# Kernel tuning notes

Hardware: AMD Instinct MI355X
Metric: run time of the kernel (lower is better)

Reference implementation:

```python
import jax, jax.numpy as jnp
import numpy as np

O = 100000   # num objects
R = 1000000  # num triplets
D = 128      # per-slot feature dim (input_dim[0]=input_dim[1]=input_dim[2])
SUM_D = 3 * D  # MLP in/out width
H = 256      # hidden_dim


def setup_inputs() -> dict:
    key = jax.random.key(0)
    k1, k2, k3, k4, k5 = jax.random.split(key, 5)
    object_feats = jax.random.normal(k1, (O, D), dtype=jnp.float32)
    relation_feats = jax.random.normal(k2, (R, D), dtype=jnp.float32)
    triplet = jax.random.randint(k3, (R, 3), 0, O, dtype=jnp.int64)
    # MLP: Linear(SUM_D->H) + ReLU + Linear(H->SUM_D), kaiming-normal init
    W1 = jax.random.normal(k4, (SUM_D, H), dtype=jnp.float32) * np.sqrt(2.0 / SUM_D)
    b1 = jnp.zeros((H,), dtype=jnp.float32)
    W2 = jax.random.normal(k5, (H, SUM_D), dtype=jnp.float32) * np.sqrt(2.0 / H)
    b2 = jnp.zeros((SUM_D,), dtype=jnp.float32)
    return {
        "object_feats": object_feats,
        "relation_feats": relation_feats,
        "W1": W1, "b1": b1, "W2": W2, "b2": b2,
        "triplet": triplet,
        "triplet_len": R,
    }


def reference(object_feats, relation_feats, W1, b1, W2, b2, triplet, triplet_len):
    t = triplet[:triplet_len]                      # [R, 3]
    subs = t[:, 0]                                 # [R]
    objs = t[:, 1]                                 # [R]
    # gather subj/obj feats, concat with relation feats -> [R, 3D]
    gcn_feat = jnp.concatenate(
        [object_feats[subs], relation_feats, object_feats[objs]], axis=1)
    # 2-layer MLP
    h = jax.nn.relu(gcn_feat @ W1 + b1)            # [R, H]
    out = h @ W2 + b2                              # [R, 3D]
    sub_out = out[:, :D]
    rel_out = out[:, D:-D]
    obj_out = out[:, -D:]
    # scatter-add back to object nodes, then mean by degree, plus residual
    acc = jnp.zeros_like(object_feats)
    acc = acc.at[subs].add(sub_out).at[objs].add(obj_out)   # [O, D]
    one = jnp.ones((triplet_len,), dtype=object_feats.dtype)
    cnt = jnp.zeros((object_feats.shape[0],), dtype=object_feats.dtype)
    cnt = cnt.at[subs].add(one).at[objs].add(one)           # [O]
    output_feat = acc / jnp.clip(cnt, 1.0)[:, None] + object_feats
    return (output_feat, rel_out, triplet, triplet_len)
```

## Files before the change

kernel.cpp:

```cpp
#include <hip/hip_runtime.h>

#define O_N 100000
#define R_N 1000000
#define DIM 128
#define SD 384
#define HD 256
#define BR 64
#define NT (R_N / BR)
#define OBJ8 (O_N * DIM / 8)

typedef __attribute__((ext_vector_type(8))) short short8;
typedef __attribute__((ext_vector_type(4))) float f32x4;

static __device__ __forceinline__ unsigned short f2bf(float x) {
    union { float f; unsigned int u; } v; v.f = x;
    unsigned int r = v.u + 0x7FFFu + ((v.u >> 16) & 1u);
    return (unsigned short)(r >> 16);
}
static __device__ __forceinline__ unsigned long long pack4(f32x4 v) {
    return  (unsigned long long)f2bf(v.x)
         | ((unsigned long long)f2bf(v.y) << 16)
         | ((unsigned long long)f2bf(v.z) << 32)
         | ((unsigned long long)f2bf(v.w) << 48);
}

__global__ void prep_weights(const float* __restrict__ W1, const float* __restrict__ W2,
                             unsigned short* __restrict__ W1T, unsigned short* __restrict__ W2T) {
    int i = blockIdx.x * 256 + threadIdx.x;
    if (i < SD * HD) {
        int h = i / SD, k = i - h * SD;
        W1T[i] = f2bf(W1[k * HD + h]);
    } else {
        int j = i - SD * HD;
        int c = j / HD, k = j - c * HD;
        W2T[j] = f2bf(W2[k * SD + c]);
    }
}

__global__ void conv_obj(const float* __restrict__ objF, unsigned short* __restrict__ objBF) {
    int i = blockIdx.x * 256 + threadIdx.x;
    if (i < OBJ8) {
        f32x4 v0 = ((const f32x4*)(objF + (size_t)i * 8))[0];
        f32x4 v1 = ((const f32x4*)(objF + (size_t)i * 8))[1];
        unsigned long long* dd = (unsigned long long*)(objBF + (size_t)i * 8);
        dd[0] = pack4(v0);
        dd[1] = pack4(v1);
    }
}

__global__ void trip_cnt(const int* __restrict__ trip, float* __restrict__ tripOut,
                         float* __restrict__ lenOut, float* __restrict__ cnt,
                         const int* __restrict__ tlen) {
    int i = blockIdx.x * 256 + threadIdx.x;
    if (i < R_N) {
        int s = trip[3 * i], o = trip[3 * i + 1], t2 = trip[3 * i + 2];
        tripOut[3 * i]     = (float)s;
        tripOut[3 * i + 1] = (float)o;
        tripOut[3 * i + 2] = (float)t2;
        atomicAdd(&cnt[min(max(s, 0), O_N - 1)], 1.0f);
        atomicAdd(&cnt[min(max(o, 0), O_N - 1)], 1.0f);
        if (i == 0) lenOut[0] = (float)tlen[0];
    }
}

__global__ __launch_bounds__(256, 3)
void mlp_kernel(const unsigned short* __restrict__ objBF, const float* __restrict__ relF,
                const unsigned short* __restrict__ W1T, const unsigned short* __restrict__ W2T,
                const float* __restrict__ b1, const float* __restrict__ b2,
                const int* __restrict__ trip,
                float* __restrict__ accB, float* __restrict__ relOut) {
    __shared__ __align__(16) unsigned char Hs[32768];
    __shared__ int idxBuf[128];

    const int tid  = threadIdx.x;
    const int lane = tid & 63;
    const int w    = tid >> 6;
    const int r0   = blockIdx.x * BR;
    const int l15  = lane & 15;
    const int l4   = lane >> 4;
    const int hW   = w * 64;
    const int cW   = w * 96;

    int subG[4], objG[4];
    #pragma unroll
    for (int nr = 0; nr < 4; ++nr) {
        int rr = r0 + nr * 16 + l15;
        subG[nr] = min(max(trip[3 * rr], 0), O_N - 1);
        objG[nr] = min(max(trip[3 * rr + 1], 0), O_N - 1);
    }

    f32x4 acc1[4][4];
    #pragma unroll
    for (int a = 0; a < 4; ++a)
        #pragma unroll
        for (int b = 0; b < 4; ++b) acc1[a][b] = (f32x4)0.0f;

    #define G1STEP(K0, BFR_EXPR)                                              \
    {                                                                         \
        const int k0 = (K0);                                                  \
        short8 af[4], bfr[4];                                                 \
        _Pragma("unroll")                                                     \
        for (int nr = 0; nr < 4; ++nr) { BFR_EXPR; }                          \
        _Pragma("unroll")                                                     \
        for (int mh = 0; mh < 4; ++mh)                                        \
            af[mh] = *(const short8*)(W1T + (hW + mh * 16 + l15) * SD + k0 + 8 * l4); \
        _Pragma("unroll")                                                     \
        for (int mh = 0; mh < 4; ++mh)                                        \
            _Pragma("unroll")                                                 \
            for (int nr = 0; nr < 4; ++nr)                                    \
                acc1[mh][nr] = __builtin_amdgcn_mfma_f32_16x16x32_bf16(       \
                    af[mh], bfr[nr], acc1[mh][nr], 0, 0, 0);                  \
    }

    #pragma unroll
    for (int ks = 0; ks < 4; ++ks)
        G1STEP(ks * 32,
            bfr[nr] = *(const short8*)(objBF + (size_t)subG[nr] * DIM + k0 + l4 * 8));
    #pragma unroll
    for (int ks = 4; ks < 8; ++ks)
        G1STEP(ks * 32,
            {
                const float* rp = relF + (size_t)(r0 + nr * 16 + l15) * DIM + (k0 - 128) + l4 * 8;
                f32x4 a0 = ((const f32x4*)rp)[0];
                f32x4 a1 = ((const f32x4*)rp)[1];
                union { unsigned long long q[2]; short8 v; } u;
                u.q[0] = pack4(a0); u.q[1] = pack4(a1);
                bfr[nr] = u.v;
            });
    #pragma unroll
    for (int ks = 8; ks < 12; ++ks)
        G1STEP(ks * 32,
            bfr[nr] = *(const short8*)(objBF + (size_t)objG[nr] * DIM + (k0 - 256) + l4 * 8));
    #undef G1STEP

    #pragma unroll
    for (int mh = 0; mh < 4; ++mh) {
        int hbase = hW + mh * 16 + 4 * l4;
        float bb0 = b1[hbase], bb1 = b1[hbase + 1], bb2 = b1[hbase + 2], bb3 = b1[hbase + 3];
        int hb   = hbase >> 3;
        int half = (hbase >> 2) & 1;
        #pragma unroll
        for (int nr = 0; nr < 4; ++nr) {
            int rel = nr * 16 + l15;
            unsigned long long pk =
                  (unsigned long long)f2bf(fmaxf(acc1[mh][nr][0] + bb0, 0.f))
                | ((unsigned long long)f2bf(fmaxf(acc1[mh][nr][1] + bb1, 0.f)) << 16)
                | ((unsigned long long)f2bf(fmaxf(acc1[mh][nr][2] + bb2, 0.f)) << 32)
                | ((unsigned long long)f2bf(fmaxf(acc1[mh][nr][3] + bb3, 0.f)) << 48);
            *(unsigned long long*)(Hs + rel * 512 + ((hb ^ (rel & 15)) << 4) + half * 8) = pk;
        }
    }
    if (tid < 2 * BR) {
        int rr = r0 + (tid & (BR - 1));
        idxBuf[tid] = min(max(trip[3 * rr + (tid >> 6)], 0), O_N - 1);
    }
    __syncthreads();

    f32x4 acc2[4][6];
    #pragma unroll
    for (int a = 0; a < 4; ++a)
        #pragma unroll
        for (int b = 0; b < 6; ++b) acc2[a][b] = (f32x4)0.0f;

    #pragma unroll
    for (int ks = 0; ks < 8; ++ks) {
        int k0 = ks * 32;
        short8 ha[4], wb[6];
        #pragma unroll
        for (int ma = 0; ma < 4; ++ma) {
            int rel = ma * 16 + l15;
            int hb  = (k0 >> 3) + l4;
            ha[ma] = *(const short8*)(Hs + rel * 512 + ((hb ^ (rel & 15)) << 4));
        }
        #pragma unroll
        for (int nb = 0; nb < 6; ++nb) {
            int c = cW + nb * 16 + l15;
            wb[nb] = *(const short8*)(W2T + c * HD + k0 + 8 * l4);
        }
        #pragma unroll
        for (int ma = 0; ma < 4; ++ma)
            #pragma unroll
            for (int nb = 0; nb < 6; ++nb)
                acc2[ma][nb] = __builtin_amdgcn_mfma_f32_16x16x32_bf16(
                    ha[ma], wb[nb], acc2[ma][nb], 0, 0, 0);
    }

    #pragma unroll
    for (int ma = 0; ma < 4; ++ma) {
        int rloc = ma * 16 + 4 * l4;
        int rg   = r0 + rloc;
        int subs[4], objs[4];
        #pragma unroll
        for (int q = 0; q < 4; ++q) {
            subs[q] = idxBuf[rloc + q];
            objs[q] = idxBuf[BR + rloc + q];
        }
        #pragma unroll
        for (int nb = 0; nb < 6; ++nb) {
            int c = cW + nb * 16 + l15;
            float b2v = b2[c];
            #pragma unroll
            for (int q = 0; q < 4; ++q) {
                float v = acc2[ma][nb][q] + b2v;
                if (c < DIM) {
                    atomicAdd(accB + (size_t)subs[q] * DIM + c, v);
                } else if (c < 2 * DIM) {
                    relOut[(size_t)(rg + q) * DIM + (c - DIM)] = v;
                } else {
                    atomicAdd(accB + (size_t)objs[q] * DIM + (c - 2 * DIM), v);
                }
            }
        }
    }
}

__global__ void finalize(const float* __restrict__ accB, const float* __restrict__ cnt,
                         const float* __restrict__ objF, float* __restrict__ outF) {
    int i = blockIdx.x * 256 + threadIdx.x;
    if (i < O_N * DIM / 4) {
        int row = i >> 5;
        float c = fmaxf(cnt[row], 1.0f);
        f32x4 a = ((const f32x4*)accB)[i];
        f32x4 o = ((const f32x4*)objF)[i];
        f32x4 r;
        r.x = a.x / c + o.x;
        r.y = a.y / c + o.y;
        r.z = a.z / c + o.z;
        r.w = a.w / c + o.w;
        ((f32x4*)outF)[i] = r;
    }
}

extern "C" void kernel_launch(void* const* d_in, const int* in_sizes, int n_in,
                              void* d_out, int out_size, void* d_ws, size_t ws_size,
                              hipStream_t stream) {
    const float* objF = (const float*)d_in[0];
    const float* relF = (const float*)d_in[1];
    const float* W1   = (const float*)d_in[2];
    const float* b1   = (const float*)d_in[3];
    const float* W2   = (const float*)d_in[4];
    const float* b2   = (const float*)d_in[5];
    const int*   trip = (const int*)d_in[6];
    const int*   tlen = (const int*)d_in[7];

    float* outF    = (float*)d_out;
    float* relOut  = outF + (size_t)O_N * DIM;
    float* tripOut = relOut + (size_t)R_N * DIM;
    float* lenOut  = tripOut + (size_t)R_N * 3;

    unsigned short* W1T = (unsigned short*)d_ws;
    unsigned short* W2T = W1T + SD * HD;
    float* accB = (float*)(W2T + SD * HD);
    float* cnt  = accB + (size_t)O_N * DIM;
    unsigned short* objBF = (unsigned short*)(cnt + O_N);

    (void)hipMemsetAsync(accB, 0, ((size_t)O_N * DIM + O_N) * sizeof(float), stream);
    prep_weights<<<(2 * SD * HD) / 256, 256, 0, stream>>>(W1, W2, W1T, W2T);
    conv_obj<<<(OBJ8 + 255) / 256, 256, 0, stream>>>(objF, objBF);
    trip_cnt<<<(R_N + 255) / 256, 256, 0, stream>>>(trip, tripOut, lenOut, cnt, tlen);
    mlp_kernel<<<NT, 256, 0, stream>>>(objBF, relF, W1T, W2T, b1, b2, trip, accB, relOut);
    finalize<<<(O_N * DIM / 4 + 255) / 256, 256, 0, stream>>>(accB, cnt, objF, outF);
}
```

Measured before the change: 1.620 ms.

## Split fused MLP into two kernels with LDS-staged gathered inputs

Splits the fused two-layer MLP kernel into gemm1 and gemm2 kernels. The bf16 hidden activations go to global memory, reusing the rel_out buffer as scratch, and are read back by the second kernel. The first kernel now stages the gathered subject/object rows into swizzled LDS with global_load_lds and stages the converted relation rows into LDS, replacing per-lane direct global loads inside the MFMA loop. The intent is to cut register pressure and improve occupancy per stage, and to make the gathers coalesced. The cost is an extra full write and read of the R×256 bf16 hidden tensor, plus one more kernel launch.

New measurement: 2.659 ms. 1.64x slower.

```diff
diff --git a/kernel.cpp b/kernel.cpp
--- a/kernel.cpp
+++ b/kernel.cpp
@@ -64,12 +64,11 @@
 }
 
 __global__ __launch_bounds__(256, 3)
-void mlp_kernel(const unsigned short* __restrict__ objBF, const float* __restrict__ relF,
-                const unsigned short* __restrict__ W1T, const unsigned short* __restrict__ W2T,
-                const float* __restrict__ b1, const float* __restrict__ b2,
-                const int* __restrict__ trip,
-                float* __restrict__ accB, float* __restrict__ relOut) {
-    __shared__ __align__(16) unsigned char Hs[32768];
+void gemm1_kernel(const unsigned short* __restrict__ objBF, const float* __restrict__ relF,
+                  const unsigned short* __restrict__ W1T, const float* __restrict__ b1,
+                  const int* __restrict__ trip, unsigned char* __restrict__ hbfB) {
+    __shared__ __align__(16) unsigned char Xso[32768];
+    __shared__ __align__(16) unsigned char Xsr[16384];
     __shared__ int idxBuf[128];
 
     const int tid  = threadIdx.x;
@@ -79,15 +78,39 @@
     const int l15  = lane & 15;
     const int l4   = lane >> 4;
     const int hW   = w * 64;
-    const int cW   = w * 96;
-
-    int subG[4], objG[4];
-    #pragma unroll
-    for (int nr = 0; nr < 4; ++nr) {
-        int rr = r0 + nr * 16 + l15;
-        subG[nr] = min(max(trip[3 * rr], 0), O_N - 1);
-        objG[nr] = min(max(trip[3 * rr + 1], 0), O_N - 1);
-    }
+
+    if (tid < 2 * BR) {
+        int rr = r0 + (tid & (BR - 1));
+        idxBuf[tid] = min(max(trip[3 * rr + (tid >> 6)], 0), O_N - 1);
+    }
+    __syncthreads();
+
+    #pragma unroll
+    for (int it = 0; it < 8; ++it) {
+        int a   = it * 256 + tid;
+        int row = a >> 5;
+        int q   = a & 31;
+        int u   = q ^ (row & 15);
+        const unsigned short* src =
+            objBF + (size_t)((q < 16) ? idxBuf[row] : idxBuf[BR + row]) * DIM + (u & 15) * 8;
+        __builtin_amdgcn_global_load_lds(
+            (const __attribute__((address_space(1))) void*)src,
+            (__attribute__((address_space(3))) void*)(Xso + it * 4096 + w * 1024),
+            16, 0, 0);
+    }
+    #pragma unroll
+    for (int it = 0; it < 4; ++it) {
+        int a2  = it * 256 + tid;
+        int row = a2 >> 4;
+        int j   = a2 & 15;
+        const float* rp = relF + (size_t)(r0 + row) * DIM + j * 8;
+        f32x4 v0 = ((const f32x4*)rp)[0];
+        f32x4 v1 = ((const f32x4*)rp)[1];
+        union { unsigned long long q[2]; short8 v; } u;
+        u.q[0] = pack4(v0); u.q[1] = pack4(v1);
+        *(short8*)(Xsr + row * 256 + ((j ^ (row & 15)) << 4)) = u.v;
+    }
+    __syncthreads();
 
     f32x4 acc1[4][4];
     #pragma unroll
@@ -95,43 +118,30 @@
         #pragma unroll
         for (int b = 0; b < 4; ++b) acc1[a][b] = (f32x4)0.0f;
 
-    #define G1STEP(K0, BFR_EXPR)                                              \
-    {                                                                         \
-        const int k0 = (K0);                                                  \
-        short8 af[4], bfr[4];                                                 \
-        _Pragma("unroll")                                                     \
-        for (int nr = 0; nr < 4; ++nr) { BFR_EXPR; }                          \
-        _Pragma("unroll")                                                     \
-        for (int mh = 0; mh < 4; ++mh)                                        \
-            af[mh] = *(const short8*)(W1T + (hW + mh * 16 + l15) * SD + k0 + 8 * l4); \
-        _Pragma("unroll")                                                     \
-        for (int mh = 0; mh < 4; ++mh)                                        \
-            _Pragma("unroll")                                                 \
-            for (int nr = 0; nr < 4; ++nr)                                    \
-                acc1[mh][nr] = __builtin_amdgcn_mfma_f32_16x16x32_bf16(       \
-                    af[mh], bfr[nr], acc1[mh][nr], 0, 0, 0);                  \
-    }
-
-    #pragma unroll
-    for (int ks = 0; ks < 4; ++ks)
-        G1STEP(ks * 32,
-            bfr[nr] = *(const short8*)(objBF + (size_t)subG[nr] * DIM + k0 + l4 * 8));
-    #pragma unroll
-    for (int ks = 4; ks < 8; ++ks)
-        G1STEP(ks * 32,
-            {
-                const float* rp = relF + (size_t)(r0 + nr * 16 + l15) * DIM + (k0 - 128) + l4 * 8;
-                f32x4 a0 = ((const f32x4*)rp)[0];
-                f32x4 a1 = ((const f32x4*)rp)[1];
-                union { unsigned long long q[2]; short8 v; } u;
-                u.q[0] = pack4(a0); u.q[1] = pack4(a1);
-                bfr[nr] = u.v;
-            });
-    #pragma unroll
-    for (int ks = 8; ks < 12; ++ks)
-        G1STEP(ks * 32,
-            bfr[nr] = *(const short8*)(objBF + (size_t)objG[nr] * DIM + (k0 - 256) + l4 * 8));
-    #undef G1STEP
+    #pragma unroll
+    for (int ks = 0; ks < 12; ++ks) {
+        int k0 = ks * 32;
+        short8 af[4], bfr[4];
+        #pragma unroll
+        for (int mh = 0; mh < 4; ++mh)
+            af[mh] = *(const short8*)(W1T + (hW + mh * 16 + l15) * SD + k0 + 8 * l4);
+        #pragma unroll
+        for (int nr = 0; nr < 4; ++nr) {
+            int rel = nr * 16 + l15;
+            int sw  = rel & 15;
+            const unsigned char* p;
+            if (ks < 4)       p = Xso + rel * 512 + (((ks * 4 + l4) ^ sw) << 4);
+            else if (ks < 8)  p = Xsr + rel * 256 + ((((ks - 4) * 4 + l4) ^ sw) << 4);
+            else              p = Xso + rel * 512 + 256 + ((((ks - 8) * 4 + l4) ^ sw) << 4);
+            bfr[nr] = *(const short8*)p;
+        }
+        #pragma unroll
+        for (int mh = 0; mh < 4; ++mh)
+            #pragma unroll
+            for (int nr = 0; nr < 4; ++nr)
+                acc1[mh][nr] = __builtin_amdgcn_mfma_f32_16x16x32_bf16(
+                    af[mh], bfr[nr], acc1[mh][nr], 0, 0, 0);
+    }
 
     #pragma unroll
     for (int mh = 0; mh < 4; ++mh) {
@@ -147,12 +157,39 @@
                 | ((unsigned long long)f2bf(fmaxf(acc1[mh][nr][1] + bb1, 0.f)) << 16)
                 | ((unsigned long long)f2bf(fmaxf(acc1[mh][nr][2] + bb2, 0.f)) << 32)
                 | ((unsigned long long)f2bf(fmaxf(acc1[mh][nr][3] + bb3, 0.f)) << 48);
-            *(unsigned long long*)(Hs + rel * 512 + ((hb ^ (rel & 15)) << 4) + half * 8) = pk;
-        }
-    }
+            *(unsigned long long*)(hbfB + (size_t)(r0 + rel) * 512
+                                   + ((hb ^ (rel & 15)) << 4) + half * 8) = pk;
+        }
+    }
+}
+
+__global__ __launch_bounds__(256, 4)
+void gemm2_kernel(const unsigned char* __restrict__ hbfB,
+                  const unsigned short* __restrict__ W2T, const float* __restrict__ b2,
+                  const int* __restrict__ trip,
+                  float* __restrict__ accB, float* __restrict__ relOut) {
+    __shared__ __align__(16) unsigned char Hs[32768];
+    __shared__ int idxBuf[128];
+
+    const int tid  = threadIdx.x;
+    const int lane = tid & 63;
+    const int w    = tid >> 6;
+    const int r0   = blockIdx.x * BR;
+    const int l15  = lane & 15;
+    const int l4   = lane >> 4;
+    const int cW   = w * 96;
+
     if (tid < 2 * BR) {
         int rr = r0 + (tid & (BR - 1));
         idxBuf[tid] = min(max(trip[3 * rr + (tid >> 6)], 0), O_N - 1);
+    }
+    #pragma unroll
+    for (int it = 0; it < 8; ++it) {
+        const unsigned char* src = hbfB + (size_t)r0 * 512 + (size_t)(it * 256 + tid) * 16;
+        __builtin_amdgcn_global_load_lds(
+            (const __attribute__((address_space(1))) void*)src,
+            (__attribute__((address_space(3))) void*)(Hs + it * 4096 + w * 1024),
+            16, 0, 0);
     }
     __syncthreads();
 
@@ -258,6 +295,7 @@
     prep_weights<<<(2 * SD * HD) / 256, 256, 0, stream>>>(W1, W2, W1T, W2T);
     conv_obj<<<(OBJ8 + 255) / 256, 256, 0, stream>>>(objF, objBF);
     trip_cnt<<<(R_N + 255) / 256, 256, 0, stream>>>(trip, tripOut, lenOut, cnt, tlen);
-    mlp_kernel<<<NT, 256, 0, stream>>>(objBF, relF, W1T, W2T, b1, b2, trip, accB, relOut);
+    gemm1_kernel<<<NT, 256, 0, stream>>>(objBF, relF, W1T, b1, trip, (unsigned char*)relOut);
+    gemm2_kernel<<<NT, 256, 0, stream>>>((const unsigned char*)relOut, W2T, b2, trip, accB, relOut);
     finalize<<<(O_N * DIM / 4 + 255) / 256, 256, 0, stream>>>(accB, cnt, objF, outF);
 }
```
